# Kernel tuning notes

Hardware: AMD Instinct MI355X
Metric: run time of the kernel (lower is better)

Reference implementation:

```python
import jax, jax.numpy as jnp
import numpy as np
from itertools import product

# problem dims
B, D = 2, 80            # batch, grid side -> 2*80^3 = 1.024M voxel slots
N = 200000
CIN, COUT = 32, 64
KV = 27                 # 3x3x3 kernel volume


def _build_rulebook():
    """Submanifold conv rulebook: in_idx[k, j] = input row whose coord equals
    coord_j + offset_k, or N (zero pad row) if that voxel is empty/out of grid."""
    rng = np.random.default_rng(0)
    total = B * D ** 3
    flat = rng.choice(total, size=N, replace=False)
    b, rem = flat // D ** 3, flat % D ** 3
    x, y, z = rem // (D * D), (rem // D) % D, rem % D
    lookup = np.full(total, N, dtype=np.int64)  # empty -> pad index N
    lookup[flat] = np.arange(N)
    rows = []
    for dx, dy, dz in product((-1, 0, 1), repeat=3):  # kernel offsets, dilation=1
        nx, ny, nz = x + dx, y + dy, z + dz
        valid = (0 <= nx) & (nx < D) & (0 <= ny) & (ny < D) & (0 <= nz) & (nz < D)
        nflat = ((b * D + nx) * D + ny) * D + nz
        rows.append(np.where(valid, lookup[np.clip(nflat, 0, total - 1)], N))
    return np.stack(rows).astype(np.int32)  # [KV, N]


def setup_inputs() -> dict:
    key = jax.random.key(0)
    k1, k2, k3 = jax.random.split(key, 3)
    stdv = 1.0 / float(np.sqrt(CIN * KV))  # matches reset_parameters
    feats = jax.random.normal(k1, (N, CIN), dtype=jnp.float32)
    weight = jax.random.uniform(k2, (KV, CIN, COUT), jnp.float32, -stdv, stdv)
    bias = jax.random.uniform(k3, (COUT,), jnp.float32, -stdv, stdv)
    in_idx = jnp.asarray(_build_rulebook())
    return {"feats": feats, "weight": weight, "bias": bias, "in_idx": in_idx}


def reference(feats, weight, bias, in_idx):
    # pad row N = zeros so missing neighbors contribute nothing
    feats_pad = jnp.concatenate(
        [feats, jnp.zeros((1, feats.shape[1]), feats.dtype)], axis=0)  # [N+1, Cin]

    def body(acc, kw):  # scan over the 27 kernel offsets: gather -> matmul -> accumulate
        idx_k, w_k = kw                       # [N] int32, [Cin, Cout]
        return acc + feats_pad[idx_k] @ w_k, None

    out0 = jnp.zeros((feats.shape[0], weight.shape[2]), feats.dtype)  # [N, Cout]
    out, _ = jax.lax.scan(body, out0, (in_idx, weight))
    return out + bias
```

## Files before the change

### kernel.cpp

```cpp
#include <hip/hip_runtime.h>
#include <cstddef>
#include <cstdint>

#define NROWS 200000
#define CIN   32
#define COUT  64
#define KV    27

typedef __attribute__((ext_vector_type(8))) short  short8;
typedef __attribute__((ext_vector_type(4))) float  f32x4;

__device__ __forceinline__ unsigned short f2bf(float x) {
  unsigned u = __builtin_bit_cast(unsigned, x);
  u += 0x7FFFu + ((u >> 16) & 1u);
  return (unsigned short)(u >> 16);
}

__global__ void prep_weight_kernel(const float* __restrict__ w,
                                   short8* __restrict__ wsB) {
  int tid = blockIdx.x * blockDim.x + threadIdx.x;
  if (tid >= KV * 4 * 64) return;
  int lane = tid & 63;
  int t    = (tid >> 6) & 3;
  int k    = tid >> 8;
  int col  = t * 16 + (lane & 15);
  int kin0 = (lane >> 4) * 8;
  short8 v;
#pragma unroll
  for (int f = 0; f < 8; ++f)
    v[f] = (short)f2bf(w[((size_t)k * CIN + kin0 + f) * COUT + col]);
  wsB[tid] = v;
}

__global__ void prep_feats_kernel(const float* __restrict__ feats,
                                  short8* __restrict__ fb) {
  int i = blockIdx.x * blockDim.x + threadIdx.x;
  const int total8 = (NROWS + 1) * CIN / 8;
  if (i >= total8) return;
  short8 v = {0, 0, 0, 0, 0, 0, 0, 0};
  if (i < NROWS * CIN / 8) {
    const f32x4* p = (const f32x4*)feats + (size_t)i * 2;
    f32x4 a = p[0], b = p[1];
#pragma unroll
    for (int f = 0; f < 4; ++f) {
      v[f]     = (short)f2bf(a[f]);
      v[4 + f] = (short)f2bf(b[f]);
    }
  }
  fb[i] = v;
}

__global__ __launch_bounds__(256)
void spconv_mfma_kernel(const unsigned short* __restrict__ featsbf,
                        const short8* __restrict__ wsB,
                        const float* __restrict__ bias,
                        const int* __restrict__ in_idx,
                        float* __restrict__ out) {
  const int bid  = blockIdx.x;
  const int xcd  = bid & 7;
  const int i    = bid >> 3;
  const int sbid = (xcd < 6) ? xcd * 98 + i : 6 * 98 + (xcd - 6) * 97 + i;

  const int lane = threadIdx.x & 63;
  const int wid  = (sbid << 2) + (int)(threadIdx.x >> 6);
  if (wid >= NROWS / 64) return;
  const int row0 = wid << 6;
  const int c16  = lane & 15;
  const int kg   = lane >> 4;
  const int koff = kg * 8;

  f32x4 acc[4][4];
#pragma unroll
  for (int t = 0; t < 4; ++t) {
    float bv = bias[t * 16 + c16];
    f32x4 bvv = {bv, bv, bv, bv};
#pragma unroll
    for (int m = 0; m < 4; ++m) acc[m][t] = bvv;
  }

  const int*    idxp = in_idx + row0 + c16;
  const short8* bp   = wsB + lane;

  for (int k = 0; k < KV; ++k) {
    int idx[4];
#pragma unroll
    for (int m = 0; m < 4; ++m)
      idx[m] = idxp[(size_t)k * NROWS + m * 16];

    short8 bfr[4];
#pragma unroll
    for (int t = 0; t < 4; ++t) bfr[t] = bp[(k * 4 + t) * 64];

    short8 afr[4];
#pragma unroll
    for (int m = 0; m < 4; ++m)
      afr[m] = *(const short8*)(featsbf + (size_t)idx[m] * CIN + koff);

#pragma unroll
    for (int m = 0; m < 4; ++m) {
      acc[m][0] = __builtin_amdgcn_mfma_f32_16x16x32_bf16(afr[m], bfr[0], acc[m][0], 0, 0, 0);
      acc[m][1] = __builtin_amdgcn_mfma_f32_16x16x32_bf16(afr[m], bfr[1], acc[m][1], 0, 0, 0);
      acc[m][2] = __builtin_amdgcn_mfma_f32_16x16x32_bf16(afr[m], bfr[2], acc[m][2], 0, 0, 0);
      acc[m][3] = __builtin_amdgcn_mfma_f32_16x16x32_bf16(afr[m], bfr[3], acc[m][3], 0, 0, 0);
    }
  }

#pragma unroll
  for (int m = 0; m < 4; ++m)
#pragma unroll
    for (int t = 0; t < 4; ++t)
#pragma unroll
      for (int r = 0; r < 4; ++r)
        out[(size_t)(row0 + m * 16 + kg * 4 + r) * COUT + t * 16 + c16] = acc[m][t][r];
}

__global__ void spconv_naive_kernel(const float* __restrict__ feats,
                                    const float* __restrict__ w,
                                    const float* __restrict__ bias,
                                    const int* __restrict__ in_idx,
                                    float* __restrict__ out) {
  int gid = blockIdx.x * blockDim.x + threadIdx.x;
  if (gid >= NROWS * COUT) return;
  int row = gid / COUT, co = gid % COUT;
  float acc = bias[co];
  for (int k = 0; k < KV; ++k) {
    int idx = in_idx[(size_t)k * NROWS + row];
    if (idx < NROWS) {
      const float* fr = feats + (size_t)idx * CIN;
      const float* wk = w + (size_t)k * CIN * COUT + co;
#pragma unroll
      for (int c = 0; c < CIN; ++c) acc += fr[c] * wk[(size_t)c * COUT];
    }
  }
  out[gid] = acc;
}

extern "C" void kernel_launch(void* const* d_in, const int* in_sizes, int n_in,
                              void* d_out, int out_size, void* d_ws, size_t ws_size,
                              hipStream_t stream) {
  const float* feats  = (const float*)d_in[0];
  const float* weight = (const float*)d_in[1];
  const float* bias   = (const float*)d_in[2];
  const int*   in_idx = (const int*)d_in[3];
  float*       out    = (float*)d_out;

  const size_t wsB_bytes = (size_t)KV * 4 * 64 * 16;
  const size_t fb_bytes  = (size_t)(NROWS + 1) * CIN * 2;
  short8*         wsB     = (short8*)d_ws;
  unsigned short* featsbf = (unsigned short*)((char*)d_ws + wsB_bytes);

  if (ws_size >= wsB_bytes + fb_bytes) {
    prep_weight_kernel<<<27, 256, 0, stream>>>(weight, wsB);
    prep_feats_kernel<<<((NROWS + 1) * CIN / 8 + 255) / 256, 256, 0, stream>>>(
        feats, (short8*)featsbf);
    const int blocks = (NROWS / 64 + 3) / 4;
    spconv_mfma_kernel<<<blocks, 256, 0, stream>>>(
        featsbf, wsB, bias, in_idx, out);
  } else {
    spconv_naive_kernel<<<(NROWS * COUT + 255) / 256, 256, 0, stream>>>(
        feats, weight, bias, in_idx, out);
  }
}
```

Baseline: 59.59 us.

## Stage rulebook indices in LDS and prefetch next offset's indices

Each wave now loads all 27 index rows for its 64 output rows with coalesced loads up front and stores them in shared memory. The main loop reads the current offset's indices from LDS and prefetches the next offset's indices, so the dependent global index load no longer sits in front of each feature gather. The XCD-aware block remapping is dropped and launch bounds now request 4 blocks per CU. The cost is 27 KB of LDS per block and a larger register live range during the initial load. That LDS size may cap occupancy below the requested 4 blocks.

```diff
diff --git a/kernel.cpp b/kernel.cpp
--- a/kernel.cpp
+++ b/kernel.cpp
@@ -2,10 +2,11 @@
 #include <cstddef>
 #include <cstdint>
 
-#define NROWS 200000
-#define CIN   32
-#define COUT  64
-#define KV    27
+#define NROWS  200000
+#define CIN    32
+#define COUT   64
+#define KV     27
+#define NWAVES (NROWS / 64)
 
 typedef __attribute__((ext_vector_type(8))) short  short8;
 typedef __attribute__((ext_vector_type(4))) float  f32x4;
@@ -50,21 +51,31 @@
   fb[i] = v;
 }
 
-__global__ __launch_bounds__(256)
+__global__ __launch_bounds__(256, 4)
 void spconv_mfma_kernel(const unsigned short* __restrict__ featsbf,
                         const short8* __restrict__ wsB,
                         const float* __restrict__ bias,
                         const int* __restrict__ in_idx,
                         float* __restrict__ out) {
-  const int bid  = blockIdx.x;
-  const int xcd  = bid & 7;
-  const int i    = bid >> 3;
-  const int sbid = (xcd < 6) ? xcd * 98 + i : 6 * 98 + (xcd - 6) * 97 + i;
+  __shared__ int sIdx[4][KV][64];
 
-  const int lane = threadIdx.x & 63;
-  const int wid  = (sbid << 2) + (int)(threadIdx.x >> 6);
-  if (wid >= NROWS / 64) return;
+  const int tid  = threadIdx.x;
+  const int lane = tid & 63;
+  const int w    = tid >> 6;
+  const int wid  = (int)blockIdx.x * 4 + w;
+  if (wid >= NWAVES) return;
   const int row0 = wid << 6;
+
+  {
+    int tmp[KV];
+#pragma unroll
+    for (int k = 0; k < KV; ++k)
+      tmp[k] = in_idx[(size_t)k * NROWS + row0 + lane];
+#pragma unroll
+    for (int k = 0; k < KV; ++k)
+      sIdx[w][k][lane] = tmp[k];
+  }
+
   const int c16  = lane & 15;
   const int kg   = lane >> 4;
   const int koff = kg * 8;
@@ -78,14 +89,16 @@
     for (int m = 0; m < 4; ++m) acc[m][t] = bvv;
   }
 
-  const int*    idxp = in_idx + row0 + c16;
-  const short8* bp   = wsB + lane;
+  const short8* bp = wsB + lane;
+
+  int idxc[4], idxn[4];
+#pragma unroll
+  for (int m = 0; m < 4; ++m) idxc[m] = sIdx[w][0][m * 16 + c16];
 
   for (int k = 0; k < KV; ++k) {
-    int idx[4];
+    const int kn = (k + 1 < KV) ? k + 1 : KV - 1;
 #pragma unroll
-    for (int m = 0; m < 4; ++m)
-      idx[m] = idxp[(size_t)k * NROWS + m * 16];
+    for (int m = 0; m < 4; ++m) idxn[m] = sIdx[w][kn][m * 16 + c16];
 
     short8 bfr[4];
 #pragma unroll
@@ -94,7 +107,7 @@
     short8 afr[4];
 #pragma unroll
     for (int m = 0; m < 4; ++m)
-      afr[m] = *(const short8*)(featsbf + (size_t)idx[m] * CIN + koff);
+      afr[m] = *(const short8*)(featsbf + (size_t)idxc[m] * CIN + koff);
 
 #pragma unroll
     for (int m = 0; m < 4; ++m) {
@@ -103,6 +116,9 @@
       acc[m][2] = __builtin_amdgcn_mfma_f32_16x16x32_bf16(afr[m], bfr[2], acc[m][2], 0, 0, 0);
       acc[m][3] = __builtin_amdgcn_mfma_f32_16x16x32_bf16(afr[m], bfr[3], acc[m][3], 0, 0, 0);
     }
+
+#pragma unroll
+    for (int m = 0; m < 4; ++m) idxc[m] = idxn[m];
   }
 
 #pragma unroll
@@ -153,7 +169,7 @@
     prep_weight_kernel<<<27, 256, 0, stream>>>(weight, wsB);
     prep_feats_kernel<<<((NROWS + 1) * CIN / 8 + 255) / 256, 256, 0, stream>>>(
         feats, (short8*)featsbf);
-    const int blocks = (NROWS / 64 + 3) / 4;
+    const int blocks = (NWAVES + 3) / 4;
     spconv_mfma_kernel<<<blocks, 256, 0, stream>>>(
         featsbf, wsB, bias, in_idx, out);
   } else {
```

Result: faster. 58.16 us (-2.4%).
